# Kernel tuning notes

Measured on AMD Instinct MI355X. Metric: run time of the kernel, lower is better.

Reference implementation:

```python
import jax, jax.numpy as jnp
import numpy as np

B, S, H = 2, 2048, 1024
E_DYN, E_FIX = 8, 1
I_DYN, I_FIX = 512, 2048
TOP_K = 4
TOP_P = 0.75
JITTER_EPS = 0.1
CAPACITY_FACTOR = 1.25
MIN_CAPACITY = 4


def setup_inputs() -> dict:
    key = jax.random.key(0)
    k = jax.random.split(key, 8)
    sc = 0.02
    return {
        "hidden_states": jax.random.normal(k[0], (B, S, H), jnp.float32),
        "gate_w": jax.random.normal(k[1], (E_DYN + E_FIX, H), jnp.float32) * sc,
        "dyn_gate_w": jax.random.normal(k[2], (E_DYN, I_DYN, H), jnp.float32) * sc,
        "dyn_up_w": jax.random.normal(k[3], (E_DYN, I_DYN, H), jnp.float32) * sc,
        "dyn_down_w": jax.random.normal(k[4], (E_DYN, H, I_DYN), jnp.float32) * sc,
        "sh_gate_w": jax.random.normal(k[5], (E_FIX, I_FIX, H), jnp.float32) * sc,
        "sh_up_w": jax.random.normal(k[6], (E_FIX, I_FIX, H), jnp.float32) * sc,
        "sh_down_w": jax.random.normal(k[7], (E_FIX, H, I_FIX), jnp.float32) * sc,
    }


def _sparse_mixer(scores):
    # Inference path of audio_sparse_expert_mixer (training=False: no gumbel noise).
    T = scores.shape[0]
    rows = jnp.arange(T)
    masked_scores = scores
    mults, sels = [], []
    for _ in range(TOP_K):  # small fixed structural loop
        thr = jnp.max(masked_scores, axis=-1, keepdims=True)          # [T,1]
        sel = jnp.argmax(masked_scores, axis=-1)                       # [T]
        factor = jnp.maximum(jnp.abs(scores), jnp.abs(thr))
        jmask = (thr - scores) / factor > 2.0 * JITTER_EPS             # bool, no grad
        gates = jax.nn.softmax(jnp.where(jmask, -jnp.inf, masked_scores), axis=-1)
        mult = jnp.take_along_axis(gates, sel[:, None], axis=-1)[:, 0]
        masked_scores = masked_scores.at[rows, sel].set(-jnp.inf)
        mults.append(mult)
        sels.append(sel)
    return jnp.stack(mults, axis=-1), jnp.stack(sels, axis=-1)        # [T,K]


def reference(hidden_states, gate_w, dyn_gate_w, dyn_up_w, dyn_down_w, sh_gate_w, sh_up_w, sh_down_w):
    Bv, Sv, Hv = hidden_states.shape
    T = Bv * Sv
    x = hidden_states.reshape(T, Hv)
    full_logits = x @ gate_w.T                                         # [T, E_DYN+E_FIX]
    dyn_logits = full_logits[:, :E_DYN]

    # audio_dynamic_expert_selection: per-token dynamic expert count via top_p
    probs = jax.nn.softmax(dyn_logits, axis=-1)
    sorted_p = jnp.sort(probs, axis=-1)[:, ::-1]
    csum = jnp.cumsum(sorted_p, axis=-1)
    dyn_k = jnp.minimum(jnp.sum(csum < TOP_P, axis=-1) + 1, TOP_K)     # [T]

    mult, sel = _sparse_mixer(dyn_logits)                              # [T,K]
    slot_valid = jnp.arange(TOP_K)[None, :] < dyn_k[:, None]
    mult = jnp.where(slot_valid, mult, 0.0)

    # dense per-expert routing weights (scatter top-k multipliers, normalize)
    rows = jnp.arange(T)
    rw = jnp.zeros((T, E_DYN), x.dtype).at[rows[:, None], sel].add(mult)
    rw = rw / jnp.sum(rw, axis=-1, keepdims=True)

    # capacity-based expert dropping (_audio_expert_capacity)
    mask_dyn = (rw > 0).astype(jnp.int32)
    cap = max(int(np.ceil(T / E_DYN * CAPACITY_FACTOR)), MIN_CAPACITY)
    mask_dyn = mask_dyn * (jnp.cumsum(mask_dyn, axis=0) <= cap)
    expert_mask = jnp.concatenate([mask_dyn, jnp.ones((T, E_FIX), jnp.int32)], axis=-1)
    maskf = expert_mask.astype(x.dtype)

    # calculate_audio_global_routing_weight + router_weight * expert_mask
    gw = jax.nn.softmax(jnp.where(expert_mask == 0, -jnp.inf, full_logits), axis=-1)
    gd = rw * jnp.sum(gw[:, :E_DYN], axis=-1, keepdims=True)
    global_w = jnp.concatenate([gd, gw[:, E_DYN:]], axis=-1) * maskf   # [T, E_DYN+E_FIX]

    # dynamic experts (SwiGLU), dense reference over all experts; mask/weights zero out drops
    g = jnp.einsum('th,eih->tei', x, dyn_gate_w)
    u = jnp.einsum('th,eih->tei', x, dyn_up_w)
    y_dyn = jnp.einsum('tei,ehi->teh', jax.nn.silu(g) * u, dyn_down_w)
    out = jnp.einsum('te,teh->th', global_w[:, :E_DYN], y_dyn)

    # shared (fixed) experts applied to all tokens
    gs = jnp.einsum('th,fih->tfi', x, sh_gate_w)
    us = jnp.einsum('th,fih->tfi', x, sh_up_w)
    y_sh = jnp.einsum('tfi,fhi->tfh', jax.nn.silu(gs) * us, sh_down_w)
    out = out + jnp.einsum('tf,tfh->th', global_w[:, E_DYN:], y_sh)

    return out.reshape(Bv, Sv, Hv)
```

## Files before the change

### kernel.cpp

```cpp
#include <hip/hip_runtime.h>
#include <cstdint>

typedef __attribute__((ext_vector_type(8))) __bf16 bf16x8;
typedef __attribute__((ext_vector_type(4))) float f32x4;

static constexpr int T_TOK = 4096;
static constexpr int HDIM  = 1024;
static constexpr int NEXP  = 9;
static constexpr int EDYN  = 8;
static constexpr int IDYN_ = 512;
static constexpr int IFIX_ = 2048;
static constexpr int CAPE  = 640;

__device__ __forceinline__ unsigned short f2bf(float f) {
  unsigned u = __float_as_uint(f);
  u += 0x7fffu + ((u >> 16) & 1u);
  return (unsigned short)(u >> 16);
}

__device__ __forceinline__ void gl_lds16(const void* g, void* l) {
  __builtin_amdgcn_global_load_lds((const __attribute__((address_space(1))) void*)g,
                                   (__attribute__((address_space(3))) void*)l,
                                   16, 0, 0);
}

static constexpr int D0 = 1048576;
static constexpr int D1 = D0 + 1048576;
static constexpr int D2 = D1 + 1048576;
static constexpr int D3 = D2 + 524288;
static constexpr int D4 = D3 + 524288;
static constexpr int D5 = D4 + 524288;
__global__ void cvt_all_kernel(const float4* __restrict__ s1,
                               const float4* __restrict__ s2, const float4* __restrict__ s3,
                               const float4* __restrict__ s4, const float4* __restrict__ s5,
                               const float4* __restrict__ s6,
                               ushort4* __restrict__ d1,
                               ushort4* __restrict__ d2, ushort4* __restrict__ d3,
                               ushort4* __restrict__ d4, ushort4* __restrict__ d5,
                               ushort4* __restrict__ d6) {
  int stride = gridDim.x * blockDim.x;
  for (int i = blockIdx.x * blockDim.x + threadIdx.x; i < D5; i += stride) {
    const float4* s; ushort4* d; int off;
    if      (i < D0) { s = s1; d = d1; off = i; }
    else if (i < D1) { s = s2; d = d2; off = i - D0; }
    else if (i < D2) { s = s3; d = d3; off = i - D1; }
    else if (i < D3) { s = s4; d = d4; off = i - D2; }
    else if (i < D4) { s = s5; d = d5; off = i - D3; }
    else             { s = s6; d = d6; off = i - D4; }
    float4 f = s[off];
    d[off] = make_ushort4(f2bf(f.x), f2bf(f.y), f2bf(f.z), f2bf(f.w));
  }
}

__global__ __launch_bounds__(256)
void logits_routing_kernel(const float* __restrict__ x, const float* __restrict__ gw,
                           unsigned short* __restrict__ xb,
                           float* __restrict__ logits, float* __restrict__ rw,
                           int* __restrict__ mask) {
  int wave = threadIdx.x >> 6, lane = threadIdx.x & 63;
  int t = blockIdx.x * 4 + wave;
  if (t >= T_TOK) return;
  const float* xr = x + (size_t)t * HDIM;
  float acc[NEXP];
#pragma unroll
  for (int e = 0; e < NEXP; ++e) acc[e] = 0.f;
#pragma unroll
  for (int half = 0; half < 2; ++half) {
    const int h0 = half * 512 + lane * 8;
    float4 a = *(const float4*)(xr + h0);
    float4 b = *(const float4*)(xr + h0 + 4);
    float v[8] = {a.x, a.y, a.z, a.w, b.x, b.y, b.z, b.w};
    union { unsigned short us[8]; uint4 u4; } pk;
#pragma unroll
    for (int j = 0; j < 8; ++j) pk.us[j] = f2bf(v[j]);
    *(uint4*)(xb + (size_t)t * HDIM + h0) = pk.u4;
#pragma unroll
    for (int e = 0; e < NEXP; ++e) {
      float s = 0.f;
#pragma unroll
      for (int j = 0; j < 8; ++j) s += v[j] * gw[e * HDIM + h0 + j];
      acc[e] += s;
    }
  }
#pragma unroll
  for (int e = 0; e < NEXP; ++e) {
    float v = acc[e];
#pragma unroll
    for (int off = 32; off > 0; off >>= 1) v += __shfl_down(v, off, 64);
    acc[e] = v;
  }
  if (lane != 0) return;
  float s[EDYN];
#pragma unroll
  for (int e = 0; e < NEXP; ++e) logits[t * NEXP + e] = acc[e];
#pragma unroll
  for (int e = 0; e < EDYN; ++e) s[e] = acc[e];

  float m = s[0];
#pragma unroll
  for (int e = 1; e < EDYN; ++e) m = fmaxf(m, s[e]);
  float p[EDYN]; float psum = 0.f;
#pragma unroll
  for (int e = 0; e < EDYN; ++e) { p[e] = expf(s[e] - m); psum += p[e]; }
#pragma unroll
  for (int e = 0; e < EDYN; ++e) p[e] /= psum;
  float sp[EDYN];
#pragma unroll
  for (int e = 0; e < EDYN; ++e) sp[e] = p[e];
  for (int i = 1; i < EDYN; ++i) {
    float key = sp[i]; int j = i - 1;
    while (j >= 0 && sp[j] < key) { sp[j + 1] = sp[j]; --j; }
    sp[j + 1] = key;
  }
  float c = 0.f; int cnt = 0;
#pragma unroll
  for (int e = 0; e < EDYN; ++e) { c += sp[e]; cnt += (c < 0.75f) ? 1 : 0; }
  int dyn_k = cnt + 1; if (dyn_k > 4) dyn_k = 4;

  float ms[EDYN];
#pragma unroll
  for (int e = 0; e < EDYN; ++e) ms[e] = s[e];
  float mult[4]; int sel[4];
  for (int k = 0; k < 4; ++k) {
    float thr = ms[0]; int am = 0;
#pragma unroll
    for (int e = 1; e < EDYN; ++e) if (ms[e] > thr) { thr = ms[e]; am = e; }
    float vals[EDYN]; float mx = -INFINITY;
#pragma unroll
    for (int e = 0; e < EDYN; ++e) {
      float factor = fmaxf(fabsf(s[e]), fabsf(thr));
      float ratio = (thr - s[e]) / factor;
      float v = (ratio > 0.2f) ? -INFINITY : ms[e];
      vals[e] = v; mx = fmaxf(mx, v);
    }
    float sum = 0.f;
#pragma unroll
    for (int e = 0; e < EDYN; ++e) sum += expf(vals[e] - mx);
    mult[k] = expf(vals[am] - mx) / sum;
    sel[k] = am;
    ms[am] = -INFINITY;
  }
  float r[EDYN];
#pragma unroll
  for (int e = 0; e < EDYN; ++e) r[e] = 0.f;
  for (int k = 0; k < 4; ++k) if (k < dyn_k) r[sel[k]] += mult[k];
  float ssum = 0.f;
#pragma unroll
  for (int e = 0; e < EDYN; ++e) ssum += r[e];
#pragma unroll
  for (int e = 0; e < EDYN; ++e) {
    float v = r[e] / ssum;
    rw[t * EDYN + e] = v;
    mask[t * EDYN + e] = (v > 0.f) ? 1 : 0;
  }
}

__global__ __launch_bounds__(1024)
void capacity_kernel(int* __restrict__ mask, int* __restrict__ tok,
                     int* __restrict__ counts) {
  const int e = blockIdx.x;
  const int tid = threadIdx.x;
  const int lane = tid & 63, wave = tid >> 6;
  __shared__ int wsum[16];
  const int t0 = tid * 4;
  int bits[4]; int c = 0;
#pragma unroll
  for (int j = 0; j < 4; ++j) { bits[j] = mask[(t0 + j) * EDYN + e]; c += bits[j]; }
  int sc = c;
#pragma unroll
  for (int off = 1; off < 64; off <<= 1) {
    int v = __shfl_up(sc, off, 64);
    if (lane >= off) sc += v;
  }
  if (lane == 63) wsum[wave] = sc;
  __syncthreads();
  int wbase = 0;
  for (int w = 0; w < wave; ++w) wbase += wsum[w];
  int pos = wbase + sc - c;
#pragma unroll
  for (int j = 0; j < 4; ++j) {
    int keep = bits[j] && (pos < CAPE);
    if (keep) tok[e * CAPE + pos] = t0 + j;
    mask[(t0 + j) * EDYN + e] = keep;
    pos += bits[j];
  }
  int total = 0;
  for (int w = 0; w < 16; ++w) total += wsum[w];
  int cnt = total < CAPE ? total : CAPE;
  if (tid == 0) counts[e] = cnt;
  for (int r = cnt + tid; r < CAPE; r += 1024) tok[e * CAPE + r] = -1;
}

__global__ __launch_bounds__(256)
void final_gate_kernel(const float* __restrict__ logits, const int* __restrict__ mask,
                       const float* __restrict__ rw, float* __restrict__ gdyn,
                       float* __restrict__ wsh) {
  int t = blockIdx.x * blockDim.x + threadIdx.x;
  if (t >= T_TOK) return;
  float vals[NEXP]; float mx = -INFINITY;
  int mk[EDYN];
#pragma unroll
  for (int e = 0; e < EDYN; ++e) {
    mk[e] = mask[t * EDYN + e];
    vals[e] = mk[e] ? logits[t * NEXP + e] : -INFINITY;
    mx = fmaxf(mx, vals[e]);
  }
  vals[EDYN] = logits[t * NEXP + EDYN];
  mx = fmaxf(mx, vals[EDYN]);
  float ex[NEXP]; float sum = 0.f;
#pragma unroll
  for (int e = 0; e < NEXP; ++e) { ex[e] = expf(vals[e] - mx); sum += ex[e]; }
  float inv = 1.f / sum;
  float sd = 0.f;
#pragma unroll
  for (int e = 0; e < EDYN; ++e) sd += ex[e] * inv;
#pragma unroll
  for (int e = 0; e < EDYN; ++e)
    gdyn[t * EDYN + e] = mk[e] ? rw[t * EDYN + e] * sd : 0.f;
  wsh[t] = ex[EDYN] * inv;
}

__global__ __launch_bounds__(512, 2)
void gemm_gateup_8ph(const unsigned short* __restrict__ xb,
                     const unsigned short* __restrict__ Wg,
                     const unsigned short* __restrict__ Wu,
                     unsigned short* __restrict__ act) {
  extern __shared__ char lds[];
  constexpr int NT = HDIM / 64;
  const int tid  = threadIdx.x;
  const int lane = tid & 63;
  const int wid  = tid >> 6;
  const int wrh  = wid >> 2;
  const int wc   = wid & 3;
  const int m0 = (blockIdx.x & 15) * 256;
  const int n0 = (blockIdx.x >> 4) * 128;

  const int srow = wid * 16 + (lane >> 2);
  const int sb9  = (lane >> 5) & 1;
  const int scl  = ((lane & 3) << 4) ^ (sb9 << 5);
  const char* sA0 = (const char*)xb + (size_t)(m0 + srow) * 2048 + scl;
  const char* sA1 = sA0 + (size_t)128 * 2048;
  const char* sBg = (const char*)Wg + (size_t)(n0 + srow) * 2048 + scl;
  const char* sBu = (const char*)Wu + (size_t)(n0 + srow) * 2048 + scl;
  const int ldsW = wid * 1024;

  const int rl  = lane & 15;
  const int swz = ((lane >> 4) << 4) ^ ((rl & 8) << 2);
  const int aRd = wrh * 16384 + rl * 64 + swz;
  const int bRd = wc * 2048 + rl * 64 + swz;

  f32x4 accg[8][2], accu[8][2];
#pragma unroll
  for (int i = 0; i < 8; ++i)
#pragma unroll
    for (int j = 0; j < 2; ++j) {
      f32x4 z = {0.f, 0.f, 0.f, 0.f};
      accg[i][j] = z; accu[i][j] = z;
    }
  bf16x8 aF[2][4][2];
  bf16x8 bF[2][2];

#define STAGE8(srcp, regoff)                                               \
  if (ktN < NT) {                                                          \
    gl_lds16((srcp) + (size_t)ktN * 128,       lds + nxt * 65536 + (regoff) + ldsW);          \
    gl_lds16((srcp) + (size_t)ktN * 128 + 64,  lds + nxt * 65536 + (regoff) + 8192 + ldsW);   \
  }
#define LOAD_A8(h)                                                         \
  _Pragma("unroll") for (int rf = 0; rf < 4; ++rf)                         \
  _Pragma("unroll") for (int ks = 0; ks < 2; ++ks)                         \
    aF[h][rf][ks] = *reinterpret_cast<const bf16x8*>(                      \
      lds + cur * 65536 + aRd + ks * 8192 + (h) * 4096 + rf * 1024);
#define LOAD_B8(off)                                                       \
  _Pragma("unroll") for (int cf = 0; cf < 2; ++cf)                         \
  _Pragma("unroll") for (int ks = 0; ks < 2; ++ks)                         \
    bF[cf][ks] = *reinterpret_cast<const bf16x8*>(                         \
      lds + cur * 65536 + (off) + bRd + ks * 8192 + cf * 1024);
#define MFMA_PH8(h, ACC)                                                   \
  __builtin_amdgcn_s_setprio(1);                                           \
  _Pragma("unroll") for (int rf = 0; rf < 4; ++rf)                         \
  _Pragma("unroll") for (int cf = 0; cf < 2; ++cf)                         \
  _Pragma("unroll") for (int ks = 0; ks < 2; ++ks)                         \
    ACC[(h) * 4 + rf][cf] = __builtin_amdgcn_mfma_f32_16x16x32_bf16(       \
        aF[h][rf][ks], bF[cf][ks], ACC[(h) * 4 + rf][cf], 0, 0, 0);        \
  __builtin_amdgcn_s_setprio(0);
#define BAR8() __builtin_amdgcn_sched_barrier(0);                          \
               __builtin_amdgcn_s_barrier();                               \
               __builtin_amdgcn_sched_barrier(0);

  {
    const int ktN = 0, nxt = 0;
    STAGE8(sA0, 0) STAGE8(sA1, 16384) STAGE8(sBg, 32768) STAGE8(sBu, 49152)
  }
  asm volatile("s_waitcnt vmcnt(0)" ::: "memory");
  BAR8()

  for (int j = 0; j < NT; ++j) {
    const int cur = j & 1, nxt = cur ^ 1, ktN = j + 1;
    STAGE8(sA0, 0)
    LOAD_A8(0)
    LOAD_B8(32768)
    MFMA_PH8(0, accg)
    BAR8()
    STAGE8(sA1, 16384)
    LOAD_A8(1)
    MFMA_PH8(1, accg)
    asm volatile("s_waitcnt vmcnt(4)" ::: "memory");
    BAR8()
    STAGE8(sBg, 32768)
    LOAD_B8(49152)
    MFMA_PH8(0, accu)
    BAR8()
    STAGE8(sBu, 49152)
    MFMA_PH8(1, accu)
    asm volatile("s_waitcnt vmcnt(2)" ::: "memory");
    BAR8()
  }

#pragma unroll
  for (int rf = 0; rf < 8; ++rf)
#pragma unroll
    for (int cf = 0; cf < 2; ++cf)
#pragma unroll
      for (int jj = 0; jj < 4; ++jj) {
        int row = m0 + wrh * 128 + (rf >> 2) * 64 + (rf & 3) * 16 + ((lane >> 4) << 2) + jj;
        int col = n0 + wc * 32 + cf * 16 + (lane & 15);
        float g = accg[rf][cf][jj], u = accu[rf][cf][jj];
        float v = (g / (1.f + __expf(-g))) * u;
        act[(size_t)row * IFIX_ + col] = f2bf(v);
      }
#undef STAGE8
#undef LOAD_A8
#undef LOAD_B8
#undef MFMA_PH8
#undef BAR8
}

__global__ __launch_bounds__(256)
void gemm_gateup_dyn(const unsigned short* __restrict__ xb,
                     const unsigned short* __restrict__ Wg,
                     const unsigned short* __restrict__ Wu,
                     unsigned short* __restrict__ act,
                     const int* __restrict__ toklist,
                     const int* __restrict__ counts,
                     int N, int K, int Mstride, int MT) {
  const int e = blockIdx.z;
  const int nid = blockIdx.x;
  const int m0 = (nid % MT) * 128;
  const int n0 = (nid / MT) * 64;
  if (m0 >= counts[e]) return;

  const unsigned short* Wg_e = Wg + (size_t)e * N * K;
  const unsigned short* Wu_e = Wu + (size_t)e * N * K;
  unsigned short* act_e = act + (size_t)e * Mstride * N;
  const int* tok_e = toklist + e * CAPE;

  __shared__ __align__(16) unsigned short As[128 * 64];
  __shared__ __align__(16) unsigned short Bgs[64 * 64];
  __shared__ __align__(16) unsigned short Bus[64 * 64];

  const int tid = threadIdx.x;
  const int lane = tid & 63;
  const int wave = tid >> 6;
  const int wr = wave >> 1, wc = wave & 1;
  const int srow = tid >> 3;
  const int scol = (tid & 7) * 8;

  const unsigned short* a_src[4];
#pragma unroll
  for (int it = 0; it < 4; ++it) {
    int r = m0 + it * 32 + srow;
    int tv = tok_e[r];
    a_src[it] = xb + (size_t)(tv < 0 ? 0 : tv) * K + scol;
  }
  const unsigned short* bg_src[2]; const unsigned short* bu_src[2];
#pragma unroll
  for (int it = 0; it < 2; ++it) {
    int r = n0 + it * 32 + srow;
    bg_src[it] = Wg_e + (size_t)r * K + scol;
    bu_src[it] = Wu_e + (size_t)r * K + scol;
  }

  f32x4 accg[4][2], accu[4][2];
#pragma unroll
  for (int i = 0; i < 4; ++i)
#pragma unroll
    for (int j = 0; j < 2; ++j) {
      f32x4 z = {0.f, 0.f, 0.f, 0.f};
      accg[i][j] = z; accu[i][j] = z;
    }

  for (int kt = 0; kt < K; kt += 64) {
#pragma unroll
    for (int it = 0; it < 4; ++it)
      gl_lds16(a_src[it] + kt, &As[it * 2048 + wave * 512]);
#pragma unroll
    for (int it = 0; it < 2; ++it) {
      gl_lds16(bg_src[it] + kt, &Bgs[it * 2048 + wave * 512]);
      gl_lds16(bu_src[it] + kt, &Bus[it * 2048 + wave * 512]);
    }
    __syncthreads();
#pragma unroll
    for (int kk = 0; kk < 2; ++kk) {
      const int ko = kk * 32 + (lane >> 4) * 8;
      bf16x8 a[4], bg[2], bu[2];
#pragma unroll
      for (int mi = 0; mi < 4; ++mi)
        a[mi] = *reinterpret_cast<const bf16x8*>(&As[(wr * 64 + mi * 16 + (lane & 15)) * 64 + ko]);
#pragma unroll
      for (int ni = 0; ni < 2; ++ni) {
        bg[ni] = *reinterpret_cast<const bf16x8*>(&Bgs[(wc * 32 + ni * 16 + (lane & 15)) * 64 + ko]);
        bu[ni] = *reinterpret_cast<const bf16x8*>(&Bus[(wc * 32 + ni * 16 + (lane & 15)) * 64 + ko]);
      }
#pragma unroll
      for (int mi = 0; mi < 4; ++mi)
#pragma unroll
        for (int ni = 0; ni < 2; ++ni) {
          accg[mi][ni] = __builtin_amdgcn_mfma_f32_16x16x32_bf16(a[mi], bg[ni], accg[mi][ni], 0, 0, 0);
          accu[mi][ni] = __builtin_amdgcn_mfma_f32_16x16x32_bf16(a[mi], bu[ni], accu[mi][ni], 0, 0, 0);
        }
    }
    __syncthreads();
  }

#pragma unroll
  for (int mi = 0; mi < 4; ++mi)
#pragma unroll
    for (int ni = 0; ni < 2; ++ni)
#pragma unroll
      for (int j = 0; j < 4; ++j) {
        int row = m0 + wr * 64 + mi * 16 + (lane >> 4) * 4 + j;
        int col = n0 + wc * 32 + ni * 16 + (lane & 15);
        float g = accg[mi][ni][j], u = accu[mi][ni][j];
        float v = (g / (1.f + __expf(-g))) * u;
        act_e[(size_t)row * N + col] = f2bf(v);
      }
}

template <bool DYN>
__global__ __launch_bounds__(256)
void gemm_down_kernel(const unsigned short* __restrict__ act,
                      const unsigned short* __restrict__ Wd,
                      float* __restrict__ out,
                      const int* __restrict__ toklist,
                      const int* __restrict__ counts,
                      const float* __restrict__ gdyn,
                      const float* __restrict__ wsh,
                      int N, int K, int Mstride, int MT) {
  const int e = blockIdx.z;
  const int nid = blockIdx.x;
  const int m0 = (nid % MT) * 128;
  const int n0 = (nid / MT) * 128;
  if (DYN) { if (m0 >= counts[e]) return; }

  const unsigned short* A_e = act + (size_t)e * Mstride * K;
  const unsigned short* Wd_e = Wd + (size_t)e * N * K;

  __shared__ __align__(16) unsigned short As[128 * 64];
  __shared__ __align__(16) unsigned short Bs[128 * 64];

  const int tid = threadIdx.x;
  const int lane = tid & 63;
  const int wave = tid >> 6;
  const int wr = wave >> 1, wc = wave & 1;
  const int srow = tid >> 3;
  const int scol = (tid & 7) * 8;

  const unsigned short* a_src[4]; const unsigned short* b_src[4];
#pragma unroll
  for (int it = 0; it < 4; ++it) {
    a_src[it] = A_e + (size_t)(m0 + it * 32 + srow) * K + scol;
    b_src[it] = Wd_e + (size_t)(n0 + it * 32 + srow) * K + scol;
  }

  f32x4 acc[4][4];
#pragma unroll
  for (int i = 0; i < 4; ++i)
#pragma unroll
    for (int j = 0; j < 4; ++j) { f32x4 z = {0.f, 0.f, 0.f, 0.f}; acc[i][j] = z; }

  for (int kt = 0; kt < K; kt += 64) {
#pragma unroll
    for (int it = 0; it < 4; ++it) {
      gl_lds16(a_src[it] + kt, &As[it * 2048 + wave * 512]);
      gl_lds16(b_src[it] + kt, &Bs[it * 2048 + wave * 512]);
    }
    __syncthreads();
#pragma unroll
    for (int kk = 0; kk < 2; ++kk) {
      const int ko = kk * 32 + (lane >> 4) * 8;
      bf16x8 a[4], b[4];
#pragma unroll
      for (int mi = 0; mi < 4; ++mi)
        a[mi] = *reinterpret_cast<const bf16x8*>(&As[(wr * 64 + mi * 16 + (lane & 15)) * 64 + ko]);
#pragma unroll
      for (int ni = 0; ni < 4; ++ni)
        b[ni] = *reinterpret_cast<const bf16x8*>(&Bs[(wc * 64 + ni * 16 + (lane & 15)) * 64 + ko]);
#pragma unroll
      for (int mi = 0; mi < 4; ++mi)
#pragma unroll
        for (int ni = 0; ni < 4; ++ni)
          acc[mi][ni] = __builtin_amdgcn_mfma_f32_16x16x32_bf16(a[mi], b[ni], acc[mi][ni], 0, 0, 0);
    }
    __syncthreads();
  }

#pragma unroll
  for (int mi = 0; mi < 4; ++mi)
#pragma unroll
    for (int ni = 0; ni < 4; ++ni)
#pragma unroll
      for (int j = 0; j < 4; ++j) {
        int row = m0 + wr * 64 + mi * 16 + (lane >> 4) * 4 + j;
        int col = n0 + wc * 64 + ni * 16 + (lane & 15);
        float v = acc[mi][ni][j];
        if (DYN) {
          int t = toklist[e * CAPE + row];
          if (t >= 0)
            atomicAdd(&out[(size_t)t * HDIM + col], gdyn[t * EDYN + e] * v);
        } else {
          out[(size_t)row * HDIM + col] = wsh[row] * v;
        }
      }
}

extern "C" void kernel_launch(void* const* d_in, const int* in_sizes, int n_in,
                              void* d_out, int out_size, void* d_ws, size_t ws_size,
                              hipStream_t stream) {
  const float* x   = (const float*)d_in[0];
  const float* gw  = (const float*)d_in[1];
  const float* wdg = (const float*)d_in[2];
  const float* wdu = (const float*)d_in[3];
  const float* wdd = (const float*)d_in[4];
  const float* wsg = (const float*)d_in[5];
  const float* wsu = (const float*)d_in[6];
  const float* wsd = (const float*)d_in[7];
  float* out = (float*)d_out;

  char* p = (char*)d_ws;
  auto alloc = [&](size_t bytes) {
    char* r = p; p += (bytes + 255) & ~(size_t)255; return r;
  };
  unsigned short* xb    = (unsigned short*)alloc((size_t)T_TOK * HDIM * 2);
  unsigned short* wdgb  = (unsigned short*)alloc((size_t)EDYN * IDYN_ * HDIM * 2);
  unsigned short* wdub  = (unsigned short*)alloc((size_t)EDYN * IDYN_ * HDIM * 2);
  unsigned short* wddb  = (unsigned short*)alloc((size_t)EDYN * HDIM * IDYN_ * 2);
  unsigned short* wsgb  = (unsigned short*)alloc((size_t)IFIX_ * HDIM * 2);
  unsigned short* wsub  = (unsigned short*)alloc((size_t)IFIX_ * HDIM * 2);
  unsigned short* wsdb  = (unsigned short*)alloc((size_t)HDIM * IFIX_ * 2);
  unsigned short* actsh = (unsigned short*)alloc((size_t)T_TOK * IFIX_ * 2);
  unsigned short* actdy = (unsigned short*)alloc((size_t)EDYN * CAPE * IDYN_ * 2);
  float* logits = (float*)alloc((size_t)T_TOK * NEXP * 4);
  float* rw     = (float*)alloc((size_t)T_TOK * EDYN * 4);
  int*   mask   = (int*)alloc((size_t)T_TOK * EDYN * 4);
  float* gdyn   = (float*)alloc((size_t)T_TOK * EDYN * 4);
  float* wshv   = (float*)alloc((size_t)T_TOK * 4);
  int*   counts = (int*)alloc(256);
  int*   tok    = (int*)alloc((size_t)EDYN * CAPE * 4);

  cvt_all_kernel<<<dim3(2048), dim3(256), 0, stream>>>(
      (const float4*)wdg, (const float4*)wdu, (const float4*)wdd,
      (const float4*)wsg, (const float4*)wsu, (const float4*)wsd,
      (ushort4*)wdgb, (ushort4*)wdub, (ushort4*)wddb,
      (ushort4*)wsgb, (ushort4*)wsub, (ushort4*)wsdb);

  logits_routing_kernel<<<dim3(T_TOK / 4), dim3(256), 0, stream>>>(x, gw, xb, logits, rw, mask);
  capacity_kernel<<<dim3(EDYN), dim3(1024), 0, stream>>>(mask, tok, counts);
  final_gate_kernel<<<dim3(T_TOK / 256), dim3(256), 0, stream>>>(logits, mask, rw, gdyn, wshv);

  gemm_gateup_8ph<<<dim3(256), dim3(512), 131072, stream>>>(xb, wsgb, wsub, actsh);
  gemm_down_kernel<false><<<dim3((T_TOK / 128) * (HDIM / 128), 1, 1), dim3(256), 0, stream>>>(
      actsh, wsdb, out, tok, counts, gdyn, wshv, HDIM, IFIX_, T_TOK, T_TOK / 128);
  gemm_gateup_dyn<<<dim3((CAPE / 128) * (IDYN_ / 64), 1, EDYN), dim3(256), 0, stream>>>(
      xb, wdgb, wdub, actdy, tok, counts, IDYN_, HDIM, CAPE, CAPE / 128);
  gemm_down_kernel<true><<<dim3((CAPE / 128) * (HDIM / 128), 1, EDYN), dim3(256), 0, stream>>>(
      actdy, wddb, out, tok, counts, gdyn, wshv, HDIM, IDYN_, CAPE, CAPE / 128);
}
```

Measured before the change: 317.6 us.

## Replace atomic scatter in dynamic down-proj with per-slot buffer and gather

The dynamic-expert down projection used to scatter weighted results into the output with float atomicAdd. It now writes unweighted per-slot results to an fp32 buffer, and a new gather kernel sums each token's routed expert rows into the output using a slot index recorded by the capacity kernel. This removes atomic contention and makes the summation order deterministic. In exchange it writes and reads back an extra buffer of about 21 MB and adds another kernel launch.

```diff
diff --git a/kernel.cpp b/kernel.cpp
--- a/kernel.cpp
+++ b/kernel.cpp
@@ -157,7 +157,7 @@
 
 __global__ __launch_bounds__(1024)
 void capacity_kernel(int* __restrict__ mask, int* __restrict__ tok,
-                     int* __restrict__ counts) {
+                     int* __restrict__ slot, int* __restrict__ counts) {
   const int e = blockIdx.x;
   const int tid = threadIdx.x;
   const int lane = tid & 63, wave = tid >> 6;
@@ -182,6 +182,7 @@
     int keep = bits[j] && (pos < CAPE);
     if (keep) tok[e * CAPE + pos] = t0 + j;
     mask[(t0 + j) * EDYN + e] = keep;
+    slot[(t0 + j) * EDYN + e] = keep ? pos : -1;
     pos += bits[j];
   }
   int total = 0;
@@ -436,24 +437,15 @@
       }
 }
 
-template <bool DYN>
 __global__ __launch_bounds__(256)
-void gemm_down_kernel(const unsigned short* __restrict__ act,
-                      const unsigned short* __restrict__ Wd,
-                      float* __restrict__ out,
-                      const int* __restrict__ toklist,
-                      const int* __restrict__ counts,
-                      const float* __restrict__ gdyn,
-                      const float* __restrict__ wsh,
-                      int N, int K, int Mstride, int MT) {
-  const int e = blockIdx.z;
+void gemm_down_sh(const unsigned short* __restrict__ act,
+                  const unsigned short* __restrict__ Wd,
+                  float* __restrict__ out,
+                  const float* __restrict__ wsh,
+                  int N, int K, int MT) {
   const int nid = blockIdx.x;
   const int m0 = (nid % MT) * 128;
   const int n0 = (nid / MT) * 128;
-  if (DYN) { if (m0 >= counts[e]) return; }
-
-  const unsigned short* A_e = act + (size_t)e * Mstride * K;
-  const unsigned short* Wd_e = Wd + (size_t)e * N * K;
 
   __shared__ __align__(16) unsigned short As[128 * 64];
   __shared__ __align__(16) unsigned short Bs[128 * 64];
@@ -468,8 +460,8 @@
   const unsigned short* a_src[4]; const unsigned short* b_src[4];
 #pragma unroll
   for (int it = 0; it < 4; ++it) {
-    a_src[it] = A_e + (size_t)(m0 + it * 32 + srow) * K + scol;
-    b_src[it] = Wd_e + (size_t)(n0 + it * 32 + srow) * K + scol;
+    a_src[it] = act + (size_t)(m0 + it * 32 + srow) * K + scol;
+    b_src[it] = Wd + (size_t)(n0 + it * 32 + srow) * K + scol;
   }
 
   f32x4 acc[4][4];
@@ -512,15 +504,103 @@
       for (int j = 0; j < 4; ++j) {
         int row = m0 + wr * 64 + mi * 16 + (lane >> 4) * 4 + j;
         int col = n0 + wc * 64 + ni * 16 + (lane & 15);
-        float v = acc[mi][ni][j];
-        if (DYN) {
-          int t = toklist[e * CAPE + row];
-          if (t >= 0)
-            atomicAdd(&out[(size_t)t * HDIM + col], gdyn[t * EDYN + e] * v);
-        } else {
-          out[(size_t)row * HDIM + col] = wsh[row] * v;
-        }
+        out[(size_t)row * HDIM + col] = wsh[row] * acc[mi][ni][j];
       }
+}
+
+__global__ __launch_bounds__(256)
+void gemm_down_dyn(const unsigned short* __restrict__ act,
+                   const unsigned short* __restrict__ Wd,
+                   float* __restrict__ ydyn,
+                   const int* __restrict__ counts,
+                   int N, int K, int MT) {
+  const int e = blockIdx.z;
+  const int nid = blockIdx.x;
+  const int m0 = (nid % MT) * 128;
+  const int n0 = (nid / MT) * 128;
+  if (m0 >= counts[e]) return;
+
+  const unsigned short* A_e = act + (size_t)e * CAPE * K;
+  const unsigned short* Wd_e = Wd + (size_t)e * N * K;
+  float* y_e = ydyn + (size_t)e * CAPE * HDIM;
+
+  __shared__ __align__(16) unsigned short As[128 * 64];
+  __shared__ __align__(16) unsigned short Bs[128 * 64];
+
+  const int tid = threadIdx.x;
+  const int lane = tid & 63;
+  const int wave = tid >> 6;
+  const int wr = wave >> 1, wc = wave & 1;
+  const int srow = tid >> 3;
+  const int scol = (tid & 7) * 8;
+
+  const unsigned short* a_src[4]; const unsigned short* b_src[4];
+#pragma unroll
+  for (int it = 0; it < 4; ++it) {
+    a_src[it] = A_e + (size_t)(m0 + it * 32 + srow) * K + scol;
+    b_src[it] = Wd_e + (size_t)(n0 + it * 32 + srow) * K + scol;
+  }
+
+  f32x4 acc[4][4];
+#pragma unroll
+  for (int i = 0; i < 4; ++i)
+#pragma unroll
+    for (int j = 0; j < 4; ++j) { f32x4 z = {0.f, 0.f, 0.f, 0.f}; acc[i][j] = z; }
+
+  for (int kt = 0; kt < K; kt += 64) {
+#pragma unroll
+    for (int it = 0; it < 4; ++it) {
+      gl_lds16(a_src[it] + kt, &As[it * 2048 + wave * 512]);
+      gl_lds16(b_src[it] + kt, &Bs[it * 2048 + wave * 512]);
+    }
+    __syncthreads();
+#pragma unroll
+    for (int kk = 0; kk < 2; ++kk) {
+      const int ko = kk * 32 + (lane >> 4) * 8;
+      bf16x8 a[4], b[4];
+#pragma unroll
+      for (int mi = 0; mi < 4; ++mi)
+        a[mi] = *reinterpret_cast<const bf16x8*>(&As[(wr * 64 + mi * 16 + (lane & 15)) * 64 + ko]);
+#pragma unroll
+      for (int ni = 0; ni < 4; ++ni)
+        b[ni] = *reinterpret_cast<const bf16x8*>(&Bs[(wc * 64 + ni * 16 + (lane & 15)) * 64 + ko]);
+#pragma unroll
+      for (int mi = 0; mi < 4; ++mi)
+#pragma unroll
+        for (int ni = 0; ni < 4; ++ni)
+          acc[mi][ni] = __builtin_amdgcn_mfma_f32_16x16x32_bf16(a[mi], b[ni], acc[mi][ni], 0, 0, 0);
+    }
+    __syncthreads();
+  }
+
+#pragma unroll
+  for (int mi = 0; mi < 4; ++mi)
+#pragma unroll
+    for (int ni = 0; ni < 4; ++ni)
+#pragma unroll
+      for (int j = 0; j < 4; ++j) {
+        int row = m0 + wr * 64 + mi * 16 + (lane >> 4) * 4 + j;
+        int col = n0 + wc * 64 + ni * 16 + (lane & 15);
+        y_e[(size_t)row * HDIM + col] = acc[mi][ni][j];
+      }
+}
+
+__global__ __launch_bounds__(256)
+void gather_kernel(const float* __restrict__ ydyn, const int* __restrict__ slot,
+                   const float* __restrict__ gdyn, float* __restrict__ out) {
+  const int t = blockIdx.x;
+  const int c = threadIdx.x * 4;
+  float4 v = *(float4*)&out[(size_t)t * HDIM + c];
+#pragma unroll
+  for (int e = 0; e < EDYN; ++e) {
+    int s = slot[t * EDYN + e];
+    if (s >= 0) {
+      float g = gdyn[t * EDYN + e];
+      float4 y = *(const float4*)&ydyn[((size_t)e * CAPE + s) * HDIM + c];
+      v.x += g * y.x; v.y += g * y.y; v.z += g * y.z; v.w += g * y.w;
+    }
+  }
+  *(float4*)&out[(size_t)t * HDIM + c] = v;
 }
 
 extern "C" void kernel_launch(void* const* d_in, const int* in_sizes, int n_in,
@@ -549,9 +629,11 @@
   unsigned short* wsdb  = (unsigned short*)alloc((size_t)HDIM * IFIX_ * 2);
   unsigned short* actsh = (unsigned short*)alloc((size_t)T_TOK * IFIX_ * 2);
   unsigned short* actdy = (unsigned short*)alloc((size_t)EDYN * CAPE * IDYN_ * 2);
+  float* ydyn   = (float*)alloc((size_t)EDYN * CAPE * HDIM * 4);
   float* logits = (float*)alloc((size_t)T_TOK * NEXP * 4);
   float* rw     = (float*)alloc((size_t)T_TOK * EDYN * 4);
   int*   mask   = (int*)alloc((size_t)T_TOK * EDYN * 4);
+  int*   slot   = (int*)alloc((size_t)T_TOK * EDYN * 4);
   float* gdyn   = (float*)alloc((size_t)T_TOK * EDYN * 4);
   float* wshv   = (float*)alloc((size_t)T_TOK * 4);
   int*   counts = (int*)alloc(256);
@@ -564,14 +646,15 @@
       (ushort4*)wsgb, (ushort4*)wsub, (ushort4*)wsdb);
 
   logits_routing_kernel<<<dim3(T_TOK / 4), dim3(256), 0, stream>>>(x, gw, xb, logits, rw, mask);
-  capacity_kernel<<<dim3(EDYN), dim3(1024), 0, stream>>>(mask, tok, counts);
+  capacity_kernel<<<dim3(EDYN), dim3(1024), 0, stream>>>(mask, tok, slot, counts);
   final_gate_kernel<<<dim3(T_TOK / 256), dim3(256), 0, stream>>>(logits, mask, rw, gdyn, wshv);
 
   gemm_gateup_8ph<<<dim3(256), dim3(512), 131072, stream>>>(xb, wsgb, wsub, actsh);
-  gemm_down_kernel<false><<<dim3((T_TOK / 128) * (HDIM / 128), 1, 1), dim3(256), 0, stream>>>(
-      actsh, wsdb, out, tok, counts, gdyn, wshv, HDIM, IFIX_, T_TOK, T_TOK / 128);
+  gemm_down_sh<<<dim3((T_TOK / 128) * (HDIM / 128), 1, 1), dim3(256), 0, stream>>>(
+      actsh, wsdb, out, wshv, HDIM, IFIX_, T_TOK / 128);
   gemm_gateup_dyn<<<dim3((CAPE / 128) * (IDYN_ / 64), 1, EDYN), dim3(256), 0, stream>>>(
       xb, wdgb, wdub, actdy, tok, counts, IDYN_, HDIM, CAPE, CAPE / 128);
-  gemm_down_kernel<true><<<dim3((CAPE / 128) * (HDIM / 128), 1, EDYN), dim3(256), 0, stream>>>(
-      actdy, wddb, out, tok, counts, gdyn, wshv, HDIM, IDYN_, CAPE, CAPE / 128);
-}
+  gemm_down_dyn<<<dim3((CAPE / 128) * (HDIM / 128), 1, EDYN), dim3(256), 0, stream>>>(
+      actdy, wddb, ydyn, counts, HDIM, IDYN_, CAPE / 128);
+  gather_kernel<<<dim3(T_TOK), dim3(256), 0, stream>>>(ydyn, slot, gdyn, out);
+}
```

Result: faster. 307.2 us (-3.3%).
